# Kernel optimization log

Measured on AMD Instinct MI355X. Metric: run time of the kernel, lower is better.

## Reference

```python
import jax, jax.numpy as jnp
import numpy as np

DIM = 256; INNER = 512; HEADS = 8; DHEAD = 64; WS = 7; K = 3; EPS = 1e-5

def _rel_idx(ws):
    idx = np.array([[x, y] for x in range(ws) for y in range(ws)])
    d = idx[None, :, :] - idx[:, None, :]
    d[:, :, 0] += ws - 1
    d[:, :, 1] += ws - 1
    d[:, :, 0] *= 2 * ws - 1
    return jnp.asarray(d.sum(-1))  # [ws^2, ws^2] int

REL_IDX = _rel_idx(WS)

def _proj(x, dw, g, b, m, v, pw):
    # depthwise conv (k=3, pad=1, groups=C) -> BN (eval mode) -> 1x1 pointwise
    p = K // 2
    y = jax.lax.conv_general_dilated(x, dw, (1, 1), ((p, p), (p, p)),
                                     feature_group_count=x.shape[1])
    y = (y - m[None, :, None, None]) * jax.lax.rsqrt(v[None, :, None, None] + EPS) \
        * g[None, :, None, None] + b[None, :, None, None]
    return jax.lax.conv_general_dilated(y, pw, (1, 1), 'VALID')

def _windows(t):
    # [b, h*d, H, W] -> [b, h, nw, ws*ws, d]  (non-shuffle partition)
    b, c, H, W = t.shape
    nh, nw = H // WS, W // WS
    t = t.reshape(b, HEADS, DHEAD, nh, WS, nw, WS)
    t = t.transpose(0, 1, 3, 5, 4, 6, 2)  # b h nh nw ws ws d
    return t.reshape(b, HEADS, nh * nw, WS * WS, DHEAD)

def _unwindows(t, H, W):
    b = t.shape[0]
    nh, nw = H // WS, W // WS
    t = t.reshape(b, HEADS, nh, nw, WS, WS, DHEAD)
    t = t.transpose(0, 1, 6, 2, 4, 3, 5)  # b h d nh ws nw ws
    return t.reshape(b, HEADS * DHEAD, H, W)

def setup_inputs() -> dict:
    key = jax.random.key(0)
    ks = jax.random.split(key, 32)
    d = {'x': jax.random.normal(ks[0], (16, DIM, 56, 56), jnp.float32)}
    i = 1
    for p in ('q', 'k', 'v'):
        d[p + '_dw'] = jax.random.normal(ks[i], (DIM, 1, K, K), jnp.float32) * 0.1; i += 1
        d[p + '_g'] = jax.random.uniform(ks[i], (DIM,), jnp.float32); i += 1
        d[p + '_b'] = jax.random.normal(ks[i], (DIM,), jnp.float32) * 0.1; i += 1
        d[p + '_m'] = jax.random.normal(ks[i], (DIM,), jnp.float32) * 0.1; i += 1
        d[p + '_v'] = jax.random.uniform(ks[i], (DIM,), jnp.float32); i += 1
        d[p + '_pw'] = jax.random.normal(ks[i], (INNER, DIM, 1, 1), jnp.float32) * 0.05; i += 1
    d['pos_emb'] = jax.random.normal(ks[i], ((2 * WS - 1) ** 2, HEADS), jnp.float32); i += 1
    d['out_w'] = jax.random.normal(ks[i], (DIM, INNER, 1, 1), jnp.float32) * 0.05; i += 1
    d['out_b'] = jax.random.normal(ks[i], (DIM,), jnp.float32) * 0.1
    return d

def reference(x, q_dw, q_g, q_b, q_m, q_v, q_pw,
              k_dw, k_g, k_b, k_m, k_v, k_pw,
              v_dw, v_g, v_b, v_m, v_v, v_pw,
              pos_emb, out_w, out_b):
    H, W = x.shape[2], x.shape[3]
    q = _windows(_proj(x, q_dw, q_g, q_b, q_m, q_v, q_pw))
    k = _windows(_proj(x, k_dw, k_g, k_b, k_m, k_v, k_pw))
    v = _windows(_proj(x, v_dw, v_g, v_b, v_m, v_v, v_pw))
    dots = jnp.einsum('bhwid,bhwjd->bhwij', q, k) * (DHEAD ** -0.5)
    bias = pos_emb[REL_IDX]              # [i, j, heads]
    dots = dots + bias.transpose(2, 0, 1)[None, :, None]  # broadcast over b, w
    attn = jax.nn.softmax(dots, axis=-1)
    out = jnp.einsum('bhwij,bhwjd->bhwid', attn, v)
    out = _unwindows(out, H, W)
    out = jax.lax.conv_general_dilated(out, out_w, (1, 1), 'VALID') \
          + out_b[None, :, None, None]
    return out
```

## Files before the change

kernel.cpp:

```cpp
#include <hip/hip_runtime.h>
#include <hip/hip_bf16.h>

typedef __hip_bfloat16 bf16;
typedef __bf16 bfv8 __attribute__((ext_vector_type(8)));
typedef float f32x4 __attribute__((ext_vector_type(4)));

constexpr int B_     = 16;
constexpr int C_     = 256;
constexpr int INNER_ = 512;
constexpr int HEADS_ = 8;
constexpr int DH_    = 64;
constexpr int HW_    = 56;
constexpr int NPIX_  = HW_ * HW_;
constexpr int WS_    = 7;
constexpr int WSQ_   = 49;
constexpr int NWIN_  = 64;

static __device__ __forceinline__ void async16(const void* g, void* l) {
    __builtin_amdgcn_global_load_lds(
        (const __attribute__((address_space(1))) unsigned int*)g,
        (__attribute__((address_space(3))) unsigned int*)l, 16, 0, 0);
}

__global__ __launch_bounds__(256) void cvt4_kernel(
    const float* __restrict__ s0, const float* __restrict__ s1,
    const float* __restrict__ s2, const float* __restrict__ s3,
    bf16* __restrict__ d) {
    int g = blockIdx.y;
    const float* s = g == 0 ? s0 : (g == 1 ? s1 : (g == 2 ? s2 : s3));
    int i = blockIdx.x * 256 + threadIdx.x;
    d[(size_t)g * (INNER_ * C_) + i] = __float2bfloat16(s[i]);
}

__global__ __launch_bounds__(256) void fold_kernel(
    const float* __restrict__ dw0, const float* __restrict__ g0,
    const float* __restrict__ b0, const float* __restrict__ m0,
    const float* __restrict__ v0,
    const float* __restrict__ dw1, const float* __restrict__ g1,
    const float* __restrict__ b1, const float* __restrict__ m1,
    const float* __restrict__ v1,
    const float* __restrict__ dw2, const float* __restrict__ g2,
    const float* __restrict__ b2, const float* __restrict__ m2,
    const float* __restrict__ v2,
    float* __restrict__ wf) {
    int p = blockIdx.x, c = threadIdx.x;
    const float* dw = p == 0 ? dw0 : (p == 1 ? dw1 : dw2);
    const float* g  = p == 0 ? g0  : (p == 1 ? g1  : g2);
    const float* bb = p == 0 ? b0  : (p == 1 ? b1  : b2);
    const float* mm = p == 0 ? m0  : (p == 1 ? m1  : m2);
    const float* vv = p == 0 ? v0  : (p == 1 ? v1  : v2);
    float s = g[c] * rsqrtf(vv[c] + 1e-5f);
    float* o = wf + (size_t)(p * 256 + c) * 12;
#pragma unroll
    for (int k = 0; k < 9; ++k) o[k] = dw[c * 9 + k] * s;
    o[9] = bb[c] - mm[c] * s;
    o[10] = 0.f; o[11] = 0.f;
}

__global__ __launch_bounds__(256) void bias_pre_kernel(
    const float* __restrict__ pos, float* __restrict__ biasf) {
    int h = blockIdx.x;
    int wv = threadIdx.x >> 6, lane = threadIdx.x & 63;
    int quad = lane >> 4, col16 = lane & 15;
    float* dst = biasf + (((size_t)h * 4 + wv) * 64 + lane) * 16;
#pragma unroll
    for (int nt = 0; nt < 4; ++nt)
#pragma unroll
        for (int r = 0; r < 4; ++r) {
            int row = wv * 16 + quad * 4 + r;
            int col = nt * 16 + col16;
            float v;
            if (col >= WSQ_) v = -1e30f;
            else if (row >= WSQ_) v = 0.f;
            else {
                int xi = row / WS_, yi = row % WS_;
                int xj = col / WS_, yj = col % WS_;
                int rel = (xj - xi + 6) * 13 + (yj - yi + 6);
                v = pos[rel * HEADS_ + h];
            }
            dst[nt * 4 + r] = v;
        }
}

__global__ __launch_bounds__(256) void dwbn3_kernel(
    const float* __restrict__ x, const float* __restrict__ wf,
    bf16* __restrict__ tq, bf16* __restrict__ tk, bf16* __restrict__ tv) {
    __shared__ float xs[3 * 64 * 61];
    int y  = blockIdx.x;
    int c0 = blockIdx.y * 64;
    int b  = blockIdx.z;
    int tid = threadIdx.x;
    for (int i = tid; i < 2688; i += 256) {
        int row = i / 896;
        int rem = i - row * 896;
        int ch = rem / 14, s = rem - ch * 14;
        int yy = y + row - 1;
        float4 v4 = make_float4(0.f, 0.f, 0.f, 0.f);
        if (yy >= 0 && yy < HW_)
            v4 = *(const float4*)(x + (size_t)(b * C_ + c0 + ch) * NPIX_
                                    + yy * HW_ + s * 4);
        float* d = xs + (row * 64 + ch) * 61 + 1 + s * 4;
        d[0] = v4.x; d[1] = v4.y; d[2] = v4.z; d[3] = v4.w;
    }
    for (int j = tid; j < 192; j += 256) {
        int row = j >> 6, ch = j & 63;
        xs[(row * 64 + ch) * 61] = 0.f;
        xs[(row * 64 + ch) * 61 + 57] = 0.f;
    }
    __syncthreads();

    int cg = tid & 31, xo = tid >> 5;
    int bcol = xo * 7;
    unsigned int pack[3][7];
#pragma unroll
    for (int ci = 0; ci < 2; ++ci) {
        int ch = cg * 2 + ci;
        float4 w[3][3];
#pragma unroll
        for (int p = 0; p < 3; ++p) {
            const float* wp = wf + (size_t)(p * 256 + c0 + ch) * 12;
            w[p][0] = *(const float4*)(wp);
            w[p][1] = *(const float4*)(wp + 4);
            w[p][2] = *(const float4*)(wp + 8);
        }
        const float* r0 = xs + ch * 61;
        const float* r1 = r0 + 64 * 61;
        const float* r2 = r1 + 64 * 61;
        float a00 = r0[bcol], a01 = r0[bcol + 1];
        float a10 = r1[bcol], a11 = r1[bcol + 1];
        float a20 = r2[bcol], a21 = r2[bcol + 1];
#pragma unroll
        for (int px = 0; px < 7; ++px) {
            float a02 = r0[bcol + px + 2];
            float a12 = r1[bcol + px + 2];
            float a22 = r2[bcol + px + 2];
#pragma unroll
            for (int p = 0; p < 3; ++p) {
                float acc = w[p][2].y
                    + w[p][0].x * a00 + w[p][0].y * a01 + w[p][0].z * a02
                    + w[p][0].w * a10 + w[p][1].x * a11 + w[p][1].y * a12
                    + w[p][1].z * a20 + w[p][1].w * a21 + w[p][2].x * a22;
                bf16 hv = __float2bfloat16(acc);
                unsigned short u; __builtin_memcpy(&u, &hv, 2);
                if (ci == 0) pack[p][px] = u;
                else         pack[p][px] |= ((unsigned int)u) << 16;
            }
            a00 = a01; a01 = a02; a10 = a11; a11 = a12; a20 = a21; a21 = a22;
        }
    }
    bf16* outs[3] = {tq, tk, tv};
    size_t pbase = ((size_t)b * NPIX_ + y * HW_ + bcol) * C_ + c0 + cg * 2;
#pragma unroll
    for (int p = 0; p < 3; ++p)
#pragma unroll
        for (int px = 0; px < 7; ++px)
            *(unsigned int*)(outs[p] + pbase + px * C_) = pack[p][px];
}

__global__ __launch_bounds__(256) void gemm_qkv_mfma(
    const bf16* __restrict__ Wbase, const bf16* __restrict__ Tbase,
    bf16* __restrict__ Qbase) {
    __shared__ __align__(16) char smem[128 * 136 * 2];
    bf16* sA = (bf16*)smem;
    bf16* sB = sA + 128 * 32;
    bf16* sC = (bf16*)smem;
    int tid = threadIdx.x;
    int c0 = blockIdx.x * 128;
    int p0 = blockIdx.y * 128;
    int zp = blockIdx.z >> 4;
    int b  = blockIdx.z & 15;
    const bf16* W = Wbase + (size_t)zp * (INNER_ * C_);
    const bf16* T = Tbase + (size_t)zp * ((size_t)B_ * NPIX_ * C_);
    bf16* Q = Qbase + (size_t)zp * ((size_t)B_ * INNER_ * NPIX_);

    int row0 = tid >> 2;
    int kc   = (tid & 3) * 8;
    int pA0 = p0 + row0;       if (pA0 > NPIX_ - 1) pA0 = NPIX_ - 1;
    int pA1 = p0 + row0 + 64;  if (pA1 > NPIX_ - 1) pA1 = NPIX_ - 1;
    const bf16* gA0 = T + ((size_t)b * NPIX_ + pA0) * 256 + kc;
    const bf16* gA1 = T + ((size_t)b * NPIX_ + pA1) * 256 + kc;
    const bf16* gB0 = W + (size_t)(c0 + row0) * 256 + kc;
    const bf16* gB1 = W + (size_t)(c0 + row0 + 64) * 256 + kc;
    char* lA = (char*)sA + tid * 16;
    char* lB = (char*)sB + tid * 16;

    int lane = tid & 63, wv = tid >> 6;
    int wm = (wv >> 1) * 64;
    int wn = (wv & 1) * 64;
    int col16 = lane & 15, quad = lane >> 4;

    f32x4 acc[4][4] = {};
    for (int k0 = 0; k0 < 256; k0 += 32) {
        async16(gA0, lA);
        async16(gA1, lA + 4096);
        async16(gB0, lB);
        async16(gB1, lB + 4096);
        gA0 += 32; gA1 += 32; gB0 += 32; gB1 += 32;
        __syncthreads();
        bfv8 af[4], bfr[4];
#pragma unroll
        for (int mt = 0; mt < 4; ++mt)
            af[mt] = *(const bfv8*)(sA + (wm + mt * 16 + col16) * 32 + quad * 8);
#pragma unroll
        for (int nt = 0; nt < 4; ++nt)
            bfr[nt] = *(const bfv8*)(sB + (wn + nt * 16 + col16) * 32 + quad * 8);
#pragma unroll
        for (int mt = 0; mt < 4; ++mt)
#pragma unroll
            for (int nt = 0; nt < 4; ++nt)
                acc[mt][nt] = __builtin_amdgcn_mfma_f32_16x16x32_bf16(
                    af[mt], bfr[nt], acc[mt][nt], 0, 0, 0);
        __syncthreads();
    }
#pragma unroll
    for (int mt = 0; mt < 4; ++mt)
#pragma unroll
        for (int nt = 0; nt < 4; ++nt) {
            f32x4 a = acc[mt][nt];
#pragma unroll
            for (int r = 0; r < 4; ++r)
                sC[(wm + mt * 16 + quad * 4 + r) * 136 + wn + nt * 16 + col16] =
                    __float2bfloat16(a[r]);
        }
    __syncthreads();
#pragma unroll
    for (int j = 0; j < 8; ++j) {
        int lin = j * 256 + tid;
        int pixl = lin >> 4, chg = lin & 15;
        int p = p0 + pixl;
        if (p < NPIX_) {
            int ch = c0 + chg * 8;
            int h = ch >> 6, d = ch & 63;
            int yy = p / HW_, xx = p % HW_;
            int wdw = (yy / WS_) * 8 + (xx / WS_);
            int j49 = (yy % WS_) * WS_ + (xx % WS_);
            bfv8 vd = *(const bfv8*)(sC + pixl * 136 + chg * 8);
            *(bfv8*)(Q + ((((size_t)b * HEADS_ + h) * NWIN_ + wdw) * WSQ_ + j49) * DH_ + d) = vd;
        }
    }
}

__global__ __launch_bounds__(256) void attn_mfma(
    const bf16* __restrict__ Q, const bf16* __restrict__ Kt,
    const bf16* __restrict__ V, const float* __restrict__ biasf,
    bf16* __restrict__ O) {
    __shared__ __align__(16) bf16 qs[64 * 72];
    __shared__ __align__(16) bf16 ks[64 * 72];
    __shared__ __align__(16) bf16 vt[64 * 72];
    __shared__ __align__(16) bf16 ps[64 * 72];
    int tid = threadIdx.x;
    int w = blockIdx.x & 63;
    int h = (blockIdx.x >> 6) & 7;
    int b = blockIdx.x >> 9;
    size_t base = (((size_t)b * HEADS_ + h) * NWIN_ + w) * (WSQ_ * DH_);

    {
        bfv8 z = {};
        bfv8* v16 = (bfv8*)vt;
        for (int c = tid; c < 576; c += 256) v16[c] = z;
    }
    __syncthreads();
    {
        bfv8 z = {};
        for (int c = tid; c < 512; c += 256) {
            int row = c >> 3, col = (c & 7) * 8;
            bfv8 vq = z, vk = z;
            if (c < 392) {
                vq = *(const bfv8*)(Q + base + c * 8);
                vk = *(const bfv8*)(Kt + base + c * 8);
            }
            *(bfv8*)(qs + row * 72 + col) = vq;
            *(bfv8*)(ks + row * 72 + col) = vk;
        }
        for (int e = tid; e < WSQ_ * DH_; e += 256) {
            int j = e >> 6, d = e & 63;
            vt[d * 72 + j] = V[base + e];
        }
    }
    __syncthreads();

    int lane = tid & 63, wv = tid >> 6;
    int band = wv * 16;
    int col16 = lane & 15, quad = lane >> 4;

    f32x4 sacc[4] = {};
    bfv8 aq0 = *(const bfv8*)(qs + (band + col16) * 72 + quad * 8);
    bfv8 aq1 = *(const bfv8*)(qs + (band + col16) * 72 + 32 + quad * 8);
#pragma unroll
    for (int nt = 0; nt < 4; ++nt) {
        bfv8 bk0 = *(const bfv8*)(ks + (nt * 16 + col16) * 72 + quad * 8);
        bfv8 bk1 = *(const bfv8*)(ks + (nt * 16 + col16) * 72 + 32 + quad * 8);
        sacc[nt] = __builtin_amdgcn_mfma_f32_16x16x32_bf16(aq0, bk0, sacc[nt], 0, 0, 0);
        sacc[nt] = __builtin_amdgcn_mfma_f32_16x16x32_bf16(aq1, bk1, sacc[nt], 0, 0, 0);
    }
    const float* bp = biasf + (((size_t)h * 4 + wv) * 64 + lane) * 16;
    f32x4 bias[4];
#pragma unroll
    for (int nt = 0; nt < 4; ++nt) bias[nt] = *(const f32x4*)(bp + nt * 4);
    float p[4][4];
    float inv[4];
#pragma unroll
    for (int r = 0; r < 4; ++r) {
        float s0 = sacc[0][r] * 0.125f + bias[0][r];
        float s1 = sacc[1][r] * 0.125f + bias[1][r];
        float s2 = sacc[2][r] * 0.125f + bias[2][r];
        float s3 = sacc[3][r] * 0.125f + bias[3][r];
        float mx = fmaxf(fmaxf(s0, s1), fmaxf(s2, s3));
        mx = fmaxf(mx, __shfl_xor(mx, 1, 16));
        mx = fmaxf(mx, __shfl_xor(mx, 2, 16));
        mx = fmaxf(mx, __shfl_xor(mx, 4, 16));
        mx = fmaxf(mx, __shfl_xor(mx, 8, 16));
        float e0 = __expf(s0 - mx), e1 = __expf(s1 - mx);
        float e2 = __expf(s2 - mx), e3 = __expf(s3 - mx);
        float sm = e0 + e1 + e2 + e3;
        sm += __shfl_xor(sm, 1, 16);
        sm += __shfl_xor(sm, 2, 16);
        sm += __shfl_xor(sm, 4, 16);
        sm += __shfl_xor(sm, 8, 16);
        p[0][r] = e0; p[1][r] = e1; p[2][r] = e2; p[3][r] = e3;
        inv[r] = 1.f / sm;
    }
#pragma unroll
    for (int nt = 0; nt < 4; ++nt)
#pragma unroll
        for (int r = 0; r < 4; ++r)
            ps[(band + quad * 4 + r) * 72 + nt * 16 + col16] = __float2bfloat16(p[nt][r]);
    f32x4 oacc[4] = {};
    bfv8 ap0 = *(const bfv8*)(ps + (band + col16) * 72 + quad * 8);
    bfv8 ap1 = *(const bfv8*)(ps + (band + col16) * 72 + 32 + quad * 8);
#pragma unroll
    for (int nt = 0; nt < 4; ++nt) {
        bfv8 bv0 = *(const bfv8*)(vt + (nt * 16 + col16) * 72 + quad * 8);
        bfv8 bv1 = *(const bfv8*)(vt + (nt * 16 + col16) * 72 + 32 + quad * 8);
        oacc[nt] = __builtin_amdgcn_mfma_f32_16x16x32_bf16(ap0, bv0, oacc[nt], 0, 0, 0);
        oacc[nt] = __builtin_amdgcn_mfma_f32_16x16x32_bf16(ap1, bv1, oacc[nt], 0, 0, 0);
    }
    int wy = w >> 3, wx = w & 7;
#pragma unroll
    for (int r = 0; r < 4; ++r) {
        int i = band + quad * 4 + r;
        if (i < WSQ_) {
            int py = wy * WS_ + i / WS_, px = wx * WS_ + i % WS_;
            size_t ob = ((size_t)b * NPIX_ + py * HW_ + px) * INNER_ + h * DH_;
            float sc = inv[r];
#pragma unroll
            for (int nt = 0; nt < 4; ++nt)
                O[ob + nt * 16 + col16] = __float2bfloat16(oacc[nt][r] * sc);
        }
    }
}

__global__ __launch_bounds__(256) void gemm_out_mfma(
    const bf16* __restrict__ W, const bf16* __restrict__ O,
    const float* __restrict__ bias, float* __restrict__ out) {
    __shared__ __align__(16) bf16 sA[128 * 32];
    __shared__ __align__(16) bf16 sB[128 * 32];
    int tid = threadIdx.x;
    int c0 = blockIdx.x * 128;
    int p0 = blockIdx.y * 128;
    int b  = blockIdx.z;

    int row0 = tid >> 2;
    int kc   = (tid & 3) * 8;
    int pB0 = p0 + row0;       if (pB0 > NPIX_ - 1) pB0 = NPIX_ - 1;
    int pB1 = p0 + row0 + 64;  if (pB1 > NPIX_ - 1) pB1 = NPIX_ - 1;
    const bf16* gA0 = W + (size_t)(c0 + row0) * 512 + kc;
    const bf16* gA1 = W + (size_t)(c0 + row0 + 64) * 512 + kc;
    const bf16* gB0 = O + ((size_t)b * NPIX_ + pB0) * 512 + kc;
    const bf16* gB1 = O + ((size_t)b * NPIX_ + pB1) * 512 + kc;
    char* lA = (char*)sA + tid * 16;
    char* lB = (char*)sB + tid * 16;

    int lane = tid & 63, wv = tid >> 6;
    int wm = (wv >> 1) * 64;
    int wn = (wv & 1) * 64;
    int col16 = lane & 15, quad = lane >> 4;

    f32x4 acc[4][4] = {};
    for (int k0 = 0; k0 < 512; k0 += 32) {
        async16(gA0, lA);
        async16(gA1, lA + 4096);
        async16(gB0, lB);
        async16(gB1, lB + 4096);
        gA0 += 32; gA1 += 32; gB0 += 32; gB1 += 32;
        __syncthreads();
        bfv8 af[4], bfr[4];
#pragma unroll
        for (int mt = 0; mt < 4; ++mt)
            af[mt] = *(const bfv8*)(sA + (wm + mt * 16 + col16) * 32 + quad * 8);
#pragma unroll
        for (int nt = 0; nt < 4; ++nt)
            bfr[nt] = *(const bfv8*)(sB + (wn + nt * 16 + col16) * 32 + quad * 8);
#pragma unroll
        for (int mt = 0; mt < 4; ++mt)
#pragma unroll
            for (int nt = 0; nt < 4; ++nt)
                acc[mt][nt] = __builtin_amdgcn_mfma_f32_16x16x32_bf16(
                    af[mt], bfr[nt], acc[mt][nt], 0, 0, 0);
        __syncthreads();
    }
#pragma unroll
    for (int mt = 0; mt < 4; ++mt) {
#pragma unroll
        for (int r = 0; r < 4; ++r) {
            int ch = c0 + wm + mt * 16 + quad * 4 + r;
            float bc = bias[ch];
#pragma unroll
            for (int nt = 0; nt < 4; ++nt) {
                int p = p0 + wn + nt * 16 + col16;
                if (p < NPIX_)
                    out[((size_t)b * C_ + ch) * NPIX_ + p] = acc[mt][nt][r] + bc;
            }
        }
    }
}

extern "C" void kernel_launch(void* const* d_in, const int* in_sizes, int n_in,
                              void* d_out, int out_size, void* d_ws, size_t ws_size,
                              hipStream_t stream) {
    (void)in_sizes; (void)n_in; (void)out_size; (void)ws_size;
    const float* x     = (const float*)d_in[0];
    const float* pos   = (const float*)d_in[19];
    const float* out_w = (const float*)d_in[20];
    const float* out_b = (const float*)d_in[21];

    size_t tElems = (size_t)B_ * NPIX_ * C_;
    size_t qElems = (size_t)B_ * INNER_ * NPIX_;
    bf16* tq = (bf16*)d_ws;
    bf16* q  = tq + 3 * tElems;
    bf16* o  = tq;
    float* wf = (float*)(q + 3 * qElems);
    bf16* wq = (bf16*)(wf + 3 * 256 * 12);
    bf16* wo = wq + 3 * (INNER_ * C_);
    float* biasf = (float*)(wo + C_ * INNER_);

    dim3 blk(256);
    dim3 gDw(HW_, 4, B_);
    dim3 gQkv(INNER_ / 128, 25, 3 * B_);
    dim3 gOut(C_ / 128, 25, B_);
    dim3 gCvt((INNER_ * C_) / 256, 4);

    fold_kernel<<<3, blk, 0, stream>>>(
        (const float*)d_in[1],  (const float*)d_in[2],  (const float*)d_in[3],
        (const float*)d_in[4],  (const float*)d_in[5],
        (const float*)d_in[7],  (const float*)d_in[8],  (const float*)d_in[9],
        (const float*)d_in[10], (const float*)d_in[11],
        (const float*)d_in[13], (const float*)d_in[14], (const float*)d_in[15],
        (const float*)d_in[16], (const float*)d_in[17], wf);
    bias_pre_kernel<<<HEADS_, blk, 0, stream>>>(pos, biasf);
    cvt4_kernel<<<gCvt, blk, 0, stream>>>(
        (const float*)d_in[6], (const float*)d_in[12], (const float*)d_in[18],
        out_w, wq);

    dwbn3_kernel<<<gDw, blk, 0, stream>>>(x, wf, tq, tq + tElems, tq + 2 * tElems);
    gemm_qkv_mfma<<<gQkv, blk, 0, stream>>>(wq, tq, q);
    attn_mfma<<<B_ * HEADS_ * NWIN_, blk, 0, stream>>>(
        q, q + qElems, q + 2 * qElems, biasf, o);
    gemm_out_mfma<<<gOut, blk, 0, stream>>>(wo, o, out_b, (float*)d_out);
}
```

Baseline: 378.1 us.

## Merge setup kernels, fold q scale into GEMM, streamline attention LDS staging

Merges the three small setup kernels (weight bf16 conversion, depthwise/BN folding, bias table) into one launch, which removes launch overhead. The 1/sqrt(d) scale moves into the Q projection epilogue, and the position bias seeds the MFMA accumulator so the softmax skips a multiply-add per score. The attention kernel reuses the Q buffer for P to cut LDS use, drops the separate V zero-fill pass and its barrier, and transposes V with 8-element vector LDS stores. Rounding Q to bf16 after scaling changes numerics slightly, and reusing qs for ps needs the added barrier after the K fragment loads.

Measured after the change: 358.2 us. 5.3% less time.

```diff
diff --git a/kernel.cpp b/kernel.cpp
--- a/kernel.cpp
+++ b/kernel.cpp
@@ -22,17 +22,10 @@
         (__attribute__((address_space(3))) unsigned int*)l, 16, 0, 0);
 }
 
-__global__ __launch_bounds__(256) void cvt4_kernel(
-    const float* __restrict__ s0, const float* __restrict__ s1,
-    const float* __restrict__ s2, const float* __restrict__ s3,
-    bf16* __restrict__ d) {
-    int g = blockIdx.y;
-    const float* s = g == 0 ? s0 : (g == 1 ? s1 : (g == 2 ? s2 : s3));
-    int i = blockIdx.x * 256 + threadIdx.x;
-    d[(size_t)g * (INNER_ * C_) + i] = __float2bfloat16(s[i]);
-}
-
-__global__ __launch_bounds__(256) void fold_kernel(
+__global__ __launch_bounds__(256) void setup_kernel(
+    const float* __restrict__ pw0, const float* __restrict__ pw1,
+    const float* __restrict__ pw2, const float* __restrict__ pw3,
+    bf16* __restrict__ wq,
     const float* __restrict__ dw0, const float* __restrict__ g0,
     const float* __restrict__ b0, const float* __restrict__ m0,
     const float* __restrict__ v0,
@@ -42,44 +35,50 @@
     const float* __restrict__ dw2, const float* __restrict__ g2,
     const float* __restrict__ b2, const float* __restrict__ m2,
     const float* __restrict__ v2,
-    float* __restrict__ wf) {
-    int p = blockIdx.x, c = threadIdx.x;
-    const float* dw = p == 0 ? dw0 : (p == 1 ? dw1 : dw2);
-    const float* g  = p == 0 ? g0  : (p == 1 ? g1  : g2);
-    const float* bb = p == 0 ? b0  : (p == 1 ? b1  : b2);
-    const float* mm = p == 0 ? m0  : (p == 1 ? m1  : m2);
-    const float* vv = p == 0 ? v0  : (p == 1 ? v1  : v2);
-    float s = g[c] * rsqrtf(vv[c] + 1e-5f);
-    float* o = wf + (size_t)(p * 256 + c) * 12;
-#pragma unroll
-    for (int k = 0; k < 9; ++k) o[k] = dw[c * 9 + k] * s;
-    o[9] = bb[c] - mm[c] * s;
-    o[10] = 0.f; o[11] = 0.f;
-}
-
-__global__ __launch_bounds__(256) void bias_pre_kernel(
+    float* __restrict__ wf,
     const float* __restrict__ pos, float* __restrict__ biasf) {
-    int h = blockIdx.x;
-    int wv = threadIdx.x >> 6, lane = threadIdx.x & 63;
-    int quad = lane >> 4, col16 = lane & 15;
-    float* dst = biasf + (((size_t)h * 4 + wv) * 64 + lane) * 16;
-#pragma unroll
-    for (int nt = 0; nt < 4; ++nt)
-#pragma unroll
-        for (int r = 0; r < 4; ++r) {
-            int row = wv * 16 + quad * 4 + r;
-            int col = nt * 16 + col16;
-            float v;
-            if (col >= WSQ_) v = -1e30f;
-            else if (row >= WSQ_) v = 0.f;
-            else {
-                int xi = row / WS_, yi = row % WS_;
-                int xj = col / WS_, yj = col % WS_;
-                int rel = (xj - xi + 6) * 13 + (yj - yi + 6);
-                v = pos[rel * HEADS_ + h];
+    int bx = blockIdx.x;
+    if (bx < 2048) {
+        int g = bx >> 9;
+        const float* s = g == 0 ? pw0 : (g == 1 ? pw1 : (g == 2 ? pw2 : pw3));
+        int i = (bx & 511) * 256 + threadIdx.x;
+        wq[(size_t)g * (INNER_ * C_) + i] = __float2bfloat16(s[i]);
+    } else if (bx < 2051) {
+        int p = bx - 2048, c = threadIdx.x;
+        const float* dw = p == 0 ? dw0 : (p == 1 ? dw1 : dw2);
+        const float* g  = p == 0 ? g0  : (p == 1 ? g1  : g2);
+        const float* bb = p == 0 ? b0  : (p == 1 ? b1  : b2);
+        const float* mm = p == 0 ? m0  : (p == 1 ? m1  : m2);
+        const float* vv = p == 0 ? v0  : (p == 1 ? v1  : v2);
+        float s = g[c] * rsqrtf(vv[c] + 1e-5f);
+        float* o = wf + (size_t)(p * 256 + c) * 12;
+#pragma unroll
+        for (int k = 0; k < 9; ++k) o[k] = dw[c * 9 + k] * s;
+        o[9] = bb[c] - mm[c] * s;
+        o[10] = 0.f; o[11] = 0.f;
+    } else {
+        int h = bx - 2051;
+        int wv = threadIdx.x >> 6, lane = threadIdx.x & 63;
+        int quad = lane >> 4, col16 = lane & 15;
+        float* dst = biasf + (((size_t)h * 4 + wv) * 64 + lane) * 16;
+#pragma unroll
+        for (int nt = 0; nt < 4; ++nt)
+#pragma unroll
+            for (int r = 0; r < 4; ++r) {
+                int row = wv * 16 + quad * 4 + r;
+                int col = nt * 16 + col16;
+                float v;
+                if (col >= WSQ_) v = -1e30f;
+                else if (row >= WSQ_) v = 0.f;
+                else {
+                    int xi = row / WS_, yi = row % WS_;
+                    int xj = col / WS_, yj = col % WS_;
+                    int rel = (xj - xi + 6) * 13 + (yj - yi + 6);
+                    v = pos[rel * HEADS_ + h];
+                }
+                dst[nt * 4 + r] = v;
             }
-            dst[nt * 4 + r] = v;
-        }
+    }
 }
 
 __global__ __launch_bounds__(256) void dwbn3_kernel(
@@ -172,6 +171,7 @@
     const bf16* W = Wbase + (size_t)zp * (INNER_ * C_);
     const bf16* T = Tbase + (size_t)zp * ((size_t)B_ * NPIX_ * C_);
     bf16* Q = Qbase + (size_t)zp * ((size_t)B_ * INNER_ * NPIX_);
+    float qscale = (zp == 0) ? 0.125f : 1.0f;
 
     int row0 = tid >> 2;
     int kc   = (tid & 3) * 8;
@@ -220,7 +220,7 @@
 #pragma unroll
             for (int r = 0; r < 4; ++r)
                 sC[(wm + mt * 16 + quad * 4 + r) * 136 + wn + nt * 16 + col16] =
-                    __float2bfloat16(a[r]);
+                    __float2bfloat16(a[r] * qscale);
         }
     __syncthreads();
 #pragma unroll
@@ -247,7 +247,7 @@
     __shared__ __align__(16) bf16 qs[64 * 72];
     __shared__ __align__(16) bf16 ks[64 * 72];
     __shared__ __align__(16) bf16 vt[64 * 72];
-    __shared__ __align__(16) bf16 ps[64 * 72];
+    bf16* ps = qs;
     int tid = threadIdx.x;
     int w = blockIdx.x & 63;
     int h = (blockIdx.x >> 6) & 7;
@@ -256,13 +256,9 @@
 
     {
         bfv8 z = {};
-        bfv8* v16 = (bfv8*)vt;
-        for (int c = tid; c < 576; c += 256) v16[c] = z;
-    }
-    __syncthreads();
-    {
-        bfv8 z = {};
-        for (int c = tid; c < 512; c += 256) {
+#pragma unroll
+        for (int it = 0; it < 2; ++it) {
+            int c = it * 256 + tid;
             int row = c >> 3, col = (c & 7) * 8;
             bfv8 vq = z, vk = z;
             if (c < 392) {
@@ -272,9 +268,24 @@
             *(bfv8*)(qs + row * 72 + col) = vq;
             *(bfv8*)(ks + row * 72 + col) = vk;
         }
-        for (int e = tid; e < WSQ_ * DH_; e += 256) {
-            int j = e >> 6, d = e & 63;
-            vt[d * 72 + j] = V[base + e];
+#pragma unroll
+        for (int it = 0; it < 2; ++it) {
+            int idx = it * 256 + tid;
+            int d = idx & 63, j8 = idx >> 6;
+            bf16 val[8];
+            if (j8 < 6) {
+#pragma unroll
+                for (int u = 0; u < 8; ++u)
+                    val[u] = V[base + (j8 * 8 + u) * 64 + d];
+            } else {
+#pragma unroll
+                for (int u = 0; u < 8; ++u) {
+                    int j = j8 * 8 + u;
+                    val[u] = (j < WSQ_) ? V[base + j * 64 + d]
+                                        : __float2bfloat16(0.f);
+                }
+            }
+            *(bfv8*)(vt + d * 72 + j8 * 8) = *(const bfv8*)val;
         }
     }
     __syncthreads();
@@ -283,28 +294,29 @@
     int band = wv * 16;
     int col16 = lane & 15, quad = lane >> 4;
 
-    f32x4 sacc[4] = {};
     bfv8 aq0 = *(const bfv8*)(qs + (band + col16) * 72 + quad * 8);
     bfv8 aq1 = *(const bfv8*)(qs + (band + col16) * 72 + 32 + quad * 8);
+    bfv8 bk[4][2];
 #pragma unroll
     for (int nt = 0; nt < 4; ++nt) {
-        bfv8 bk0 = *(const bfv8*)(ks + (nt * 16 + col16) * 72 + quad * 8);
-        bfv8 bk1 = *(const bfv8*)(ks + (nt * 16 + col16) * 72 + 32 + quad * 8);
-        sacc[nt] = __builtin_amdgcn_mfma_f32_16x16x32_bf16(aq0, bk0, sacc[nt], 0, 0, 0);
-        sacc[nt] = __builtin_amdgcn_mfma_f32_16x16x32_bf16(aq1, bk1, sacc[nt], 0, 0, 0);
-    }
+        bk[nt][0] = *(const bfv8*)(ks + (nt * 16 + col16) * 72 + quad * 8);
+        bk[nt][1] = *(const bfv8*)(ks + (nt * 16 + col16) * 72 + 32 + quad * 8);
+    }
+    __syncthreads();
+
     const float* bp = biasf + (((size_t)h * 4 + wv) * 64 + lane) * 16;
-    f32x4 bias[4];
-#pragma unroll
-    for (int nt = 0; nt < 4; ++nt) bias[nt] = *(const f32x4*)(bp + nt * 4);
+    f32x4 sacc[4];
+#pragma unroll
+    for (int nt = 0; nt < 4; ++nt) {
+        sacc[nt] = *(const f32x4*)(bp + nt * 4);
+        sacc[nt] = __builtin_amdgcn_mfma_f32_16x16x32_bf16(aq0, bk[nt][0], sacc[nt], 0, 0, 0);
+        sacc[nt] = __builtin_amdgcn_mfma_f32_16x16x32_bf16(aq1, bk[nt][1], sacc[nt], 0, 0, 0);
+    }
     float p[4][4];
     float inv[4];
 #pragma unroll
     for (int r = 0; r < 4; ++r) {
-        float s0 = sacc[0][r] * 0.125f + bias[0][r];
-        float s1 = sacc[1][r] * 0.125f + bias[1][r];
-        float s2 = sacc[2][r] * 0.125f + bias[2][r];
-        float s3 = sacc[3][r] * 0.125f + bias[3][r];
+        float s0 = sacc[0][r], s1 = sacc[1][r], s2 = sacc[2][r], s3 = sacc[3][r];
         float mx = fmaxf(fmaxf(s0, s1), fmaxf(s2, s3));
         mx = fmaxf(mx, __shfl_xor(mx, 1, 16));
         mx = fmaxf(mx, __shfl_xor(mx, 2, 16));
@@ -438,19 +450,17 @@
     dim3 gDw(HW_, 4, B_);
     dim3 gQkv(INNER_ / 128, 25, 3 * B_);
     dim3 gOut(C_ / 128, 25, B_);
-    dim3 gCvt((INNER_ * C_) / 256, 4);
-
-    fold_kernel<<<3, blk, 0, stream>>>(
+
+    setup_kernel<<<2059, blk, 0, stream>>>(
+        (const float*)d_in[6], (const float*)d_in[12], (const float*)d_in[18],
+        out_w, wq,
         (const float*)d_in[1],  (const float*)d_in[2],  (const float*)d_in[3],
         (const float*)d_in[4],  (const float*)d_in[5],
         (const float*)d_in[7],  (const float*)d_in[8],  (const float*)d_in[9],
         (const float*)d_in[10], (const float*)d_in[11],
         (const float*)d_in[13], (const float*)d_in[14], (const float*)d_in[15],
-        (const float*)d_in[16], (const float*)d_in[17], wf);
-    bias_pre_kernel<<<HEADS_, blk, 0, stream>>>(pos, biasf);
-    cvt4_kernel<<<gCvt, blk, 0, stream>>>(
-        (const float*)d_in[6], (const float*)d_in[12], (const float*)d_in[18],
-        out_w, wq);
+        (const float*)d_in[16], (const float*)d_in[17], wf,
+        pos, biasf);
 
     dwbn3_kernel<<<gDw, blk, 0, stream>>>(x, wf, tq, tq + tElems, tq + 2 * tElems);
     gemm_qkv_mfma<<<gQkv, blk, 0, stream>>>(wq, tq, q);
```
